# Performance work log

Hardware: AMD Instinct MI355X
Metric: run time of the kernel (lower is better)

## Reference

```python
import jax, jax.numpy as jnp
import numpy as np

N_NODES = 100000
N_EDGES = 400000
IN_DIM = 771
HID = 256
N_GRAPHS = 64
EPS = 1e-5


def setup_inputs() -> dict:
    key = jax.random.key(0)
    ks = jax.random.split(key, 24)
    x = jax.random.normal(ks[0], (N_NODES, IN_DIM), dtype=jnp.float32)
    edge_index = jax.random.randint(ks[1], (2, N_EDGES), 0, N_NODES, dtype=jnp.int64)
    batch = jnp.sort(jax.random.randint(ks[2], (N_NODES,), 0, N_GRAPHS, dtype=jnp.int64))
    inp = {"x": x, "edge_index": edge_index, "batch": batch}
    dims = [IN_DIM, HID, HID]
    ki = 3
    for i, din in enumerate(dims):
        s = 1.0 / np.sqrt(din)
        inp[f"Wl{i}"] = jax.random.normal(ks[ki], (din, HID), dtype=jnp.float32) * s; ki += 1
        inp[f"bl{i}"] = jnp.zeros((HID,), dtype=jnp.float32)
        inp[f"Wr{i}"] = jax.random.normal(ks[ki], (din, HID), dtype=jnp.float32) * s; ki += 1
        inp[f"g{i}"] = jnp.ones((HID,), dtype=jnp.float32)
        inp[f"b{i}"] = jnp.zeros((HID,), dtype=jnp.float32)
    # attention pooling: Linear(HID, HID//2) -> Tanh -> Linear(HID//2, 1)
    inp["Wa1"] = jax.random.normal(ks[ki], (HID, HID // 2), dtype=jnp.float32) * (1.0 / np.sqrt(HID)); ki += 1
    inp["ba1"] = jnp.zeros((HID // 2,), dtype=jnp.float32)
    inp["Wa2"] = jax.random.normal(ks[ki], (HID // 2, 1), dtype=jnp.float32) * (1.0 / np.sqrt(HID // 2)); ki += 1
    inp["ba2"] = jnp.zeros((1,), dtype=jnp.float32)
    # classifier: Linear(HID, HID//2) -> ReLU -> Linear(HID//2, 1)
    inp["Wc1"] = jax.random.normal(ks[ki], (HID, HID // 2), dtype=jnp.float32) * (1.0 / np.sqrt(HID)); ki += 1
    inp["bc1"] = jnp.zeros((HID // 2,), dtype=jnp.float32)
    inp["Wc2"] = jax.random.normal(ks[ki], (HID // 2, 1), dtype=jnp.float32) * (1.0 / np.sqrt(HID // 2)); ki += 1
    inp["bc2"] = jnp.zeros((1,), dtype=jnp.float32)
    return inp


def _sage_layer(h, src, dst, Wl, bl, Wr, g, b):
    # SAGEConv(aggr='mean'): out = lin_l(mean_{j->i} x_j) + lin_r(x_i)
    msum = jax.ops.segment_sum(h[src], dst, num_segments=N_NODES)  # [N, d]
    deg = jax.ops.segment_sum(jnp.ones((src.shape[0],), h.dtype), dst, num_segments=N_NODES)
    agg = msum / jnp.maximum(deg, 1.0)[:, None]
    out = agg @ Wl + bl + h @ Wr
    # BatchNorm1d (training-mode batch stats), eval dropout (identity)
    mean = out.mean(axis=0)
    var = out.var(axis=0)
    out = (out - mean) * jax.lax.rsqrt(var + EPS) * g + b
    return jax.nn.relu(out)


def reference(x, edge_index, batch,
              Wl0, bl0, Wr0, g0, b0,
              Wl1, bl1, Wr1, g1, b1,
              Wl2, bl2, Wr2, g2, b2,
              Wa1, ba1, Wa2, ba2,
              Wc1, bc1, Wc2, bc2):
    src, dst = edge_index[0], edge_index[1]
    h = _sage_layer(x, src, dst, Wl0, bl0, Wr0, g0, b0)
    h = _sage_layer(h, src, dst, Wl1, bl1, Wr1, g1, b1)
    h = _sage_layer(h, src, dst, Wl2, bl2, Wr2, g2, b2)
    # attention pooling: per-graph softmax over node scores, weighted sum
    s = (jnp.tanh(h @ Wa1 + ba1) @ Wa2 + ba2)[:, 0]  # [N]
    smax = jax.ops.segment_max(s, batch, num_segments=N_GRAPHS)
    e = jnp.exp(s - smax[batch])
    denom = jax.ops.segment_sum(e, batch, num_segments=N_GRAPHS)
    w = e / denom[batch]
    pooled = jax.ops.segment_sum(h * w[:, None], batch, num_segments=N_GRAPHS)  # [G, HID]
    out = jax.nn.relu(pooled @ Wc1 + bc1) @ Wc2 + bc2  # [G, 1]
    return out[:, 0]
```

## Files before the change

### kernel.cpp

```cpp
#include <hip/hip_runtime.h>
#include <math.h>
#include <stdint.h>

#define HID 256
#define NGRAPH 64
typedef unsigned short ushort_t;

typedef __attribute__((ext_vector_type(8))) short short8;
typedef __attribute__((ext_vector_type(4))) float f32x4;

__device__ __forceinline__ void split2(float v, ushort_t& h, ushort_t& l) {
  unsigned u = __float_as_uint(v);
  unsigned hr = u + 0x7FFFu + ((u >> 16) & 1u);
  h = (ushort_t)(hr >> 16);
  float hf = __uint_as_float(((unsigned)h) << 16);
  float r = v - hf;
  unsigned u2 = __float_as_uint(r);
  unsigned lr = u2 + 0x7FFFu + ((u2 >> 16) & 1u);
  l = (ushort_t)(lr >> 16);
}

#define GLDS(g, l) \
  __builtin_amdgcn_global_load_lds((const __attribute__((address_space(1))) void*)(g), \
                                   (__attribute__((address_space(3))) void*)(l), 16, 0, 0)

__global__ __launch_bounds__(256) void mfma_gemm512_kernel(
    const ushort_t* __restrict__ Ah, const ushort_t* __restrict__ Al,
    const ushort_t* __restrict__ Bh, const ushort_t* __restrict__ Bl,
    float* __restrict__ C, int Mrows, int Kpad) {
  __shared__ ushort_t lAh[128 * 32];
  __shared__ ushort_t lAl[128 * 32];
  __shared__ ushort_t lBh[128 * 32];
  __shared__ ushort_t lBl[128 * 32];
  const int tid = threadIdx.x;
  const int m0 = blockIdx.y * 128;
  const int n0 = blockIdx.x * 128;
  const int w = tid >> 6, lane = tid & 63;
  const int wm = (w >> 1) * 64, wn = (w & 1) * 64;
  const int col = lane & 15, quad = lane >> 4;

  f32x4 acc[4][4];
#pragma unroll
  for (int i = 0; i < 4; ++i)
#pragma unroll
    for (int j = 0; j < 4; ++j) acc[i][j] = (f32x4)(0.f);

  for (int kt = 0; kt < Kpad; kt += 32) {
#pragma unroll
    for (int j = 0; j < 2; ++j) {
      const int ch = tid + j * 256;
      const int r = ch >> 2, c = ch & 3;
      const size_t goA = (size_t)(m0 + r) * Kpad + kt + c * 8;
      const size_t goB = (size_t)(n0 + r) * Kpad + kt + c * 8;
      GLDS(Ah + goA, &lAh[ch * 8]);
      GLDS(Al + goA, &lAl[ch * 8]);
      GLDS(Bh + goB, &lBh[ch * 8]);
      GLDS(Bl + goB, &lBl[ch * 8]);
    }
    __syncthreads();
    short8 ah[4], al[4], bh[4], bl[4];
#pragma unroll
    for (int i = 0; i < 4; ++i) {
      const int ar = wm + i * 16 + col;
      ah[i] = *(const short8*)&lAh[ar * 32 + quad * 8];
      al[i] = *(const short8*)&lAl[ar * 32 + quad * 8];
      const int br = wn + i * 16 + col;
      bh[i] = *(const short8*)&lBh[br * 32 + quad * 8];
      bl[i] = *(const short8*)&lBl[br * 32 + quad * 8];
    }
    __syncthreads();
#pragma unroll
    for (int i = 0; i < 4; ++i)
#pragma unroll
      for (int j = 0; j < 4; ++j) {
        acc[i][j] = __builtin_amdgcn_mfma_f32_16x16x32_bf16(ah[i], bh[j], acc[i][j], 0, 0, 0);
        acc[i][j] = __builtin_amdgcn_mfma_f32_16x16x32_bf16(ah[i], bl[j], acc[i][j], 0, 0, 0);
        acc[i][j] = __builtin_amdgcn_mfma_f32_16x16x32_bf16(al[i], bh[j], acc[i][j], 0, 0, 0);
      }
  }
#pragma unroll
  for (int i = 0; i < 4; ++i) {
    const int r0 = m0 + wm + i * 16 + quad * 4;
#pragma unroll
    for (int j = 0; j < 4; ++j) {
      const int cc = n0 + wn + j * 16 + col;
#pragma unroll
      for (int r = 0; r < 4; ++r)
        if (r0 + r < Mrows) C[(size_t)(r0 + r) * 512 + cc] = acc[i][j][r];
    }
  }
}

__global__ __launch_bounds__(256) void mfma_att_kernel(
    const ushort_t* __restrict__ Ah, const ushort_t* __restrict__ Al,
    const ushort_t* __restrict__ Bh, const ushort_t* __restrict__ Bl,
    const float* __restrict__ ba1, const float* __restrict__ Wa2,
    const float* __restrict__ ba2, float* __restrict__ S, int Mrows, int Kpad) {
  __shared__ ushort_t lAh[128 * 32];
  __shared__ ushort_t lAl[128 * 32];
  __shared__ ushort_t lBh[128 * 32];
  __shared__ ushort_t lBl[128 * 32];
  __shared__ float sat[128][2];
  const int tid = threadIdx.x;
  const int m0 = blockIdx.y * 128;
  const int w = tid >> 6, lane = tid & 63;
  const int wm = (w >> 1) * 64, wn = (w & 1) * 64;
  const int col = lane & 15, quad = lane >> 4;

  f32x4 acc[4][4];
#pragma unroll
  for (int i = 0; i < 4; ++i)
#pragma unroll
    for (int j = 0; j < 4; ++j) acc[i][j] = (f32x4)(0.f);

  for (int kt = 0; kt < Kpad; kt += 32) {
#pragma unroll
    for (int j = 0; j < 2; ++j) {
      const int ch = tid + j * 256;
      const int r = ch >> 2, c = ch & 3;
      const size_t goA = (size_t)(m0 + r) * Kpad + kt + c * 8;
      const size_t goB = (size_t)r * Kpad + kt + c * 8;
      GLDS(Ah + goA, &lAh[ch * 8]);
      GLDS(Al + goA, &lAl[ch * 8]);
      GLDS(Bh + goB, &lBh[ch * 8]);
      GLDS(Bl + goB, &lBl[ch * 8]);
    }
    __syncthreads();
    short8 ah[4], al[4], bh[4], bl[4];
#pragma unroll
    for (int i = 0; i < 4; ++i) {
      const int ar = wm + i * 16 + col;
      ah[i] = *(const short8*)&lAh[ar * 32 + quad * 8];
      al[i] = *(const short8*)&lAl[ar * 32 + quad * 8];
      const int br = wn + i * 16 + col;
      bh[i] = *(const short8*)&lBh[br * 32 + quad * 8];
      bl[i] = *(const short8*)&lBl[br * 32 + quad * 8];
    }
    __syncthreads();
#pragma unroll
    for (int i = 0; i < 4; ++i)
#pragma unroll
      for (int j = 0; j < 4; ++j) {
        acc[i][j] = __builtin_amdgcn_mfma_f32_16x16x32_bf16(ah[i], bh[j], acc[i][j], 0, 0, 0);
        acc[i][j] = __builtin_amdgcn_mfma_f32_16x16x32_bf16(ah[i], bl[j], acc[i][j], 0, 0, 0);
        acc[i][j] = __builtin_amdgcn_mfma_f32_16x16x32_bf16(al[i], bh[j], acc[i][j], 0, 0, 0);
      }
  }
  float part[4][4];
#pragma unroll
  for (int i = 0; i < 4; ++i)
#pragma unroll
    for (int r = 0; r < 4; ++r) part[i][r] = 0.f;
#pragma unroll
  for (int j = 0; j < 4; ++j) {
    const int cc = wn + j * 16 + col;
    const float a1 = ba1[cc];
    const float w2 = Wa2[cc];
#pragma unroll
    for (int i = 0; i < 4; ++i)
#pragma unroll
      for (int r = 0; r < 4; ++r)
        part[i][r] += tanhf(acc[i][j][r] + a1) * w2;
  }
#pragma unroll
  for (int mask = 1; mask < 16; mask <<= 1)
#pragma unroll
    for (int i = 0; i < 4; ++i)
#pragma unroll
      for (int r = 0; r < 4; ++r) part[i][r] += __shfl_xor(part[i][r], mask, 64);
  if (col == 0) {
#pragma unroll
    for (int i = 0; i < 4; ++i)
#pragma unroll
      for (int r = 0; r < 4; ++r) sat[wm + i * 16 + quad * 4 + r][wn >> 6] = part[i][r];
  }
  __syncthreads();
  if (tid < 128) {
    const int gm = m0 + tid;
    if (gm < Mrows) S[gm] = sat[tid][0] + sat[tid][1] + ba2[0];
  }
}

__global__ __launch_bounds__(256) void convert_x_kernel(
    const float* __restrict__ x, int nrows,
    ushort_t* __restrict__ xh, ushort_t* __restrict__ xl, int K, int Kpad) {
  const int perRow = Kpad / 4;
  const int t = blockIdx.x * blockDim.x + threadIdx.x;
  if (t >= nrows * perRow) return;
  const int r = t / perRow, k0 = (t % perRow) * 4;
  const float* xr = x + (size_t)r * K;
  ushort_t h[4], l[4];
#pragma unroll
  for (int i = 0; i < 4; ++i) {
    const float v = (k0 + i < K) ? xr[k0 + i] : 0.f;
    split2(v, h[i], l[i]);
  }
  const size_t o = (size_t)r * Kpad + k0;
  *(ushort4*)(xh + o) = make_ushort4(h[0], h[1], h[2], h[3]);
  *(ushort4*)(xl + o) = make_ushort4(l[0], l[1], l[2], l[3]);
}

__global__ void convert_wt_kernel(const float* __restrict__ W1, const float* __restrict__ W2,
                                  ushort_t* __restrict__ wth, ushort_t* __restrict__ wtl,
                                  int K, int Kpad, int ntot, int ld) {
  const int t = blockIdx.x * blockDim.x + threadIdx.x;
  if (t >= ntot * Kpad) return;
  const int n = t / Kpad, k = t % Kpad;
  float v = 0.f;
  if (k < K) v = (n < 256) ? W1[(size_t)k * ld + n] : W2[(size_t)k * ld + (n - 256)];
  ushort_t h, l;
  split2(v, h, l);
  wth[t] = h;
  wtl[t] = l;
}

__global__ void deg_count_kernel(const int* __restrict__ dst, int* __restrict__ degi, int nE) {
  int e = blockIdx.x * blockDim.x + threadIdx.x;
  if (e < nE) atomicAdd(&degi[dst[e]], 1);
}

__global__ __launch_bounds__(1024) void scan_kernel(const int* __restrict__ degi,
                                                    int* __restrict__ rowptr, int M) {
  __shared__ int part[1024];
  const int t = threadIdx.x;
  const int chunk = (M + 1023) / 1024;
  const int b0 = min(t * chunk, M);
  const int b1 = min(b0 + chunk, M);
  int s = 0;
  for (int i = b0; i < b1; ++i) s += degi[i];
  part[t] = s;
  __syncthreads();
  for (int off = 1; off < 1024; off <<= 1) {
    int v = (t >= off) ? part[t - off] : 0;
    __syncthreads();
    part[t] += v;
    __syncthreads();
  }
  int ex = (t == 0) ? 0 : part[t - 1];
  for (int i = b0; i < b1; ++i) {
    rowptr[i] = ex;
    ex += degi[i];
  }
  if (t == 1023) rowptr[M] = part[1023];
}

__global__ void fill_kernel(const int* __restrict__ src, const int* __restrict__ dst,
                            int* __restrict__ fill, const int* __restrict__ rowptr,
                            int* __restrict__ csr_src, int nE) {
  int e = blockIdx.x * blockDim.x + threadIdx.x;
  if (e >= nE) return;
  const int d = dst[e];
  const int pos = rowptr[d] + atomicAdd(&fill[d], 1);
  csr_src[pos] = src[e];
}

#define GNB 64
__global__ __launch_bounds__(256) void gather_combine_kernel(
    const float* __restrict__ gbuf,
    const int* __restrict__ rowptr, const int* __restrict__ csr_src,
    const float* __restrict__ bl, float* preBN,
    float* __restrict__ bsum, float* __restrict__ bsumsq, int M) {
  __shared__ float lsum[4][HID];
  __shared__ float lsq[4][HID];
  const int w = threadIdx.x >> 6;
  const int lane = threadIdx.x & 63;
  const float4 blv = ((const float4*)bl)[lane];
  float4 s = make_float4(0.f, 0.f, 0.f, 0.f);
  float4 q = make_float4(0.f, 0.f, 0.f, 0.f);
  const int base = blockIdx.x * GNB;
  for (int it = 0; it < GNB / 4; ++it) {
    const int n = base + it * 4 + w;
    if (n < M) {
      const int e0 = rowptr[n], e1 = rowptr[n + 1];
      float4 acc = make_float4(0.f, 0.f, 0.f, 0.f);
      for (int e = e0; e < e1; ++e) {
        const int sn = csr_src[e];
        const float4 v = ((const float4*)(gbuf + (size_t)sn * 512))[lane];
        acc.x += v.x; acc.y += v.y; acc.z += v.z; acc.w += v.w;
      }
      const float rd = 1.0f / fmaxf((float)(e1 - e0), 1.0f);
      const float4 hv = ((const float4*)(gbuf + (size_t)n * 512 + 256))[lane];
      float4 o;
      o.x = fmaf(acc.x, rd, blv.x + hv.x);
      o.y = fmaf(acc.y, rd, blv.y + hv.y);
      o.z = fmaf(acc.z, rd, blv.z + hv.z);
      o.w = fmaf(acc.w, rd, blv.w + hv.w);
      ((float4*)(preBN + (size_t)n * HID))[lane] = o;
      s.x += o.x; s.y += o.y; s.z += o.z; s.w += o.w;
      q.x = fmaf(o.x, o.x, q.x); q.y = fmaf(o.y, o.y, q.y);
      q.z = fmaf(o.z, o.z, q.z); q.w = fmaf(o.w, o.w, q.w);
    }
  }
  *(float4*)&lsum[w][lane * 4] = s;
  *(float4*)&lsq[w][lane * 4] = q;
  __syncthreads();
  const int c = threadIdx.x;
  const float ts = lsum[0][c] + lsum[1][c] + lsum[2][c] + lsum[3][c];
  const float tq = lsq[0][c] + lsq[1][c] + lsq[2][c] + lsq[3][c];
  atomicAdd(&bsum[c], ts);
  atomicAdd(&bsumsq[c], tq);
}

__global__ __launch_bounds__(256) void bn_apply_relu_convert_kernel(
    const float* __restrict__ preBN, const float* __restrict__ bsum,
    const float* __restrict__ bsumsq, const float* __restrict__ g, const float* __restrict__ b,
    ushort_t* __restrict__ hh, ushort_t* __restrict__ hl, float* __restrict__ hout,
    int M, int n4) {
  __shared__ float s_sc[HID], s_sh[HID];
  {
    const int c = threadIdx.x;
    const float inv = 1.0f / (float)M;
    const float mean = bsum[c] * inv;
    const float var = bsumsq[c] * inv - mean * mean;
    const float sc = g[c] * rsqrtf(var + 1e-5f);
    s_sc[c] = sc;
    s_sh[c] = b[c] - mean * sc;
  }
  __syncthreads();
  const int i = blockIdx.x * blockDim.x + threadIdx.x;
  if (i >= n4) return;
  const int c0 = (i & (HID / 4 - 1)) * 4;
  const float4 v = ((const float4*)preBN)[i];
  float o[4];
  o[0] = fmaxf(fmaf(v.x, s_sc[c0 + 0], s_sh[c0 + 0]), 0.f);
  o[1] = fmaxf(fmaf(v.y, s_sc[c0 + 1], s_sh[c0 + 1]), 0.f);
  o[2] = fmaxf(fmaf(v.z, s_sc[c0 + 2], s_sh[c0 + 2]), 0.f);
  o[3] = fmaxf(fmaf(v.w, s_sc[c0 + 3], s_sh[c0 + 3]), 0.f);
  ushort_t h[4], l[4];
#pragma unroll
  for (int k = 0; k < 4; ++k) split2(o[k], h[k], l[k]);
  ((ushort4*)hh)[i] = make_ushort4(h[0], h[1], h[2], h[3]);
  ((ushort4*)hl)[i] = make_ushort4(l[0], l[1], l[2], l[3]);
  if (hout) ((float4*)hout)[i] = make_float4(o[0], o[1], o[2], o[3]);
}

__device__ __forceinline__ unsigned fflip(float f) {
  unsigned u = __float_as_uint(f);
  return (u & 0x80000000u) ? ~u : (u | 0x80000000u);
}
__device__ __forceinline__ float funflip(unsigned u) {
  return __uint_as_float((u & 0x80000000u) ? (u ^ 0x80000000u) : ~u);
}

__global__ void seg_max_kernel(const float* __restrict__ s, const int* __restrict__ batch,
                               unsigned* __restrict__ gmax, int M) {
  __shared__ unsigned lmax[NGRAPH];
  if (threadIdx.x < NGRAPH) lmax[threadIdx.x] = 0u;
  __syncthreads();
  for (int i = blockIdx.x * blockDim.x + threadIdx.x; i < M; i += gridDim.x * blockDim.x)
    atomicMax(&lmax[batch[i]], fflip(s[i]));
  __syncthreads();
  if (threadIdx.x < NGRAPH && lmax[threadIdx.x] != 0u) atomicMax(&gmax[threadIdx.x], lmax[threadIdx.x]);
}

__global__ void seg_expsum_kernel(const float* __restrict__ s, const int* __restrict__ batch,
                                  const unsigned* __restrict__ gmax, float* __restrict__ e,
                                  float* __restrict__ denom, int M) {
  __shared__ float ld[NGRAPH];
  if (threadIdx.x < NGRAPH) ld[threadIdx.x] = 0.f;
  __syncthreads();
  for (int i = blockIdx.x * blockDim.x + threadIdx.x; i < M; i += gridDim.x * blockDim.x) {
    const int b = batch[i];
    const float v = expf(s[i] - funflip(gmax[b]));
    e[i] = v;
    atomicAdd(&ld[b], v);
  }
  __syncthreads();
  if (threadIdx.x < NGRAPH && ld[threadIdx.x] != 0.f) atomicAdd(&denom[threadIdx.x], ld[threadIdx.x]);
}

#define PNB 16
__global__ __launch_bounds__(256) void pool_kernel(
    const float* __restrict__ h, const float* __restrict__ e, const float* __restrict__ denom,
    const int* __restrict__ batch, float* __restrict__ pooled, int M) {
  const int wid = (blockIdx.x * blockDim.x + threadIdx.x) >> 6;
  const int lane = threadIdx.x & 63;
  const int n0 = wid * PNB;
  if (n0 >= M) return;
  const int n1 = min(n0 + PNB, M);
  float4 acc = make_float4(0.f, 0.f, 0.f, 0.f);
  int cur = batch[n0];
  for (int n = n0; n < n1; ++n) {
    const int b = batch[n];
    if (b != cur) {
      float* o = pooled + (size_t)cur * HID + lane * 4;
      atomicAdd(o + 0, acc.x); atomicAdd(o + 1, acc.y);
      atomicAdd(o + 2, acc.z); atomicAdd(o + 3, acc.w);
      acc = make_float4(0.f, 0.f, 0.f, 0.f);
      cur = b;
    }
    const float w = e[n] / denom[b];
    const float4 v = ((const float4*)(h + (size_t)n * HID))[lane];
    acc.x = fmaf(v.x, w, acc.x); acc.y = fmaf(v.y, w, acc.y);
    acc.z = fmaf(v.z, w, acc.z); acc.w = fmaf(v.w, w, acc.w);
  }
  float* o = pooled + (size_t)cur * HID + lane * 4;
  atomicAdd(o + 0, acc.x); atomicAdd(o + 1, acc.y);
  atomicAdd(o + 2, acc.z); atomicAdd(o + 3, acc.w);
}

__global__ __launch_bounds__(128) void classifier_kernel(
    const float* __restrict__ pooled, const float* __restrict__ Wc1, const float* __restrict__ bc1,
    const float* __restrict__ Wc2, const float* __restrict__ bc2, float* __restrict__ out) {
  __shared__ float red[128];
  const int g = blockIdx.x;
  const int j = threadIdx.x;
  float acc = bc1[j];
  const float* p = pooled + (size_t)g * HID;
  for (int c = 0; c < HID; ++c) acc = fmaf(p[c], Wc1[c * 128 + j], acc);
  red[j] = fmaxf(acc, 0.f) * Wc2[j];
  __syncthreads();
  for (int off = 64; off > 0; off >>= 1) {
    if (j < off) red[j] += red[j + off];
    __syncthreads();
  }
  if (j == 0) out[g] = red[0] + bc2[0];
}

extern "C" void kernel_launch(void* const* d_in, const int* in_sizes, int n_in,
                              void* d_out, int out_size, void* d_ws, size_t ws_size,
                              hipStream_t stream) {
  const float* x = (const float*)d_in[0];
  const int* edge = (const int*)d_in[1];
  const int* batch = (const int*)d_in[2];
  const int M = in_sizes[2];
  const int nE = in_sizes[1] / 2;
  const int IN_DIM = in_sizes[0] / M;
  const int* src = edge;
  const int* dst = edge + nE;

  const int Mpad = ((M + 127) / 128) * 128;
  const int KP0 = ((IN_DIM + 31) / 32) * 32;
  const int mblocks = (M + 127) / 128;

  float* ws = (float*)d_ws;
  float* gbuf = ws;
  float* pbuf = gbuf + (size_t)M * 512;
  float* h32 = pbuf + (size_t)M * HID;
  float* ssc = h32 + (size_t)M * HID;
  float* ew = ssc + M;
  float* bsumA = ew + M;
  unsigned* gmax = (unsigned*)(bsumA + 6 * HID);
  float* denom = (float*)(gmax + NGRAPH);
  float* pooled = denom + NGRAPH;
  int* degi = (int*)(pooled + (size_t)NGRAPH * HID);
  int* filla = degi + M;
  int* rowptr = filla + M;
  int* csr_src = rowptr + M + 1;

  ushort_t* wp = (ushort_t*)(((uintptr_t)(csr_src + nE) + 15) & ~(uintptr_t)15);
  ushort_t* w0h = wp;                 ushort_t* w0l = w0h + (size_t)512 * KP0;
  ushort_t* w1h = w0l + (size_t)512 * KP0;  ushort_t* w1l = w1h + (size_t)512 * HID;
  ushort_t* w2h = w1l + (size_t)512 * HID;  ushort_t* w2l = w2h + (size_t)512 * HID;
  ushort_t* wah = w2l + (size_t)512 * HID;  ushort_t* wal = wah + (size_t)128 * HID;
  ushort_t* cvh = (ushort_t*)(((uintptr_t)(wal + (size_t)128 * HID) + 15) & ~(uintptr_t)15);
  ushort_t* cvl = cvh + (size_t)Mpad * KP0;

  hipMemsetAsync(degi, 0, (size_t)(2 * M) * sizeof(int), stream);
  deg_count_kernel<<<(nE + 255) / 256, 256, 0, stream>>>(dst, degi, nE);
  scan_kernel<<<1, 1024, 0, stream>>>(degi, rowptr, M);
  fill_kernel<<<(nE + 255) / 256, 256, 0, stream>>>(src, dst, filla, rowptr, csr_src, nE);
  hipMemsetAsync(bsumA, 0, (size_t)(6 * HID + 2 * NGRAPH + NGRAPH * HID) * 4, stream);

  {
    const int nt0 = 512 * KP0;
    convert_wt_kernel<<<(nt0 + 255) / 256, 256, 0, stream>>>(
        (const float*)d_in[3], (const float*)d_in[5], w0h, w0l, IN_DIM, KP0, 512, HID);
    const int nt1 = 512 * HID;
    convert_wt_kernel<<<(nt1 + 255) / 256, 256, 0, stream>>>(
        (const float*)d_in[8], (const float*)d_in[10], w1h, w1l, HID, HID, 512, HID);
    convert_wt_kernel<<<(nt1 + 255) / 256, 256, 0, stream>>>(
        (const float*)d_in[13], (const float*)d_in[15], w2h, w2l, HID, HID, 512, HID);
    convert_wt_kernel<<<(128 * HID + 255) / 256, 256, 0, stream>>>(
        (const float*)d_in[18], nullptr, wah, wal, HID, HID, 128, 128);
  }

  {
    const int nt = M * (KP0 / 4);
    convert_x_kernel<<<(nt + 255) / 256, 256, 0, stream>>>(x, M, cvh, cvl, IN_DIM, KP0);
  }

  const int n4 = (int)((size_t)M * HID / 4);
  const ushort_t* WH[3] = {w0h, w1h, w2h};
  const ushort_t* WL[3] = {w0l, w1l, w2l};
  for (int l = 0; l < 3; ++l) {
    const int KP = (l == 0) ? KP0 : HID;
    const float* bl = (const float*)d_in[3 + l * 5 + 1];
    const float* gg = (const float*)d_in[3 + l * 5 + 3];
    const float* bb = (const float*)d_in[3 + l * 5 + 4];
    float* bsum = bsumA + l * 512;
    float* bsumsq = bsum + HID;

    dim3 g(4, mblocks);
    mfma_gemm512_kernel<<<g, 256, 0, stream>>>(cvh, cvl, WH[l], WL[l], gbuf, M, KP);
    gather_combine_kernel<<<(M + GNB - 1) / GNB, 256, 0, stream>>>(
        gbuf, rowptr, csr_src, bl, pbuf, bsum, bsumsq, M);
    bn_apply_relu_convert_kernel<<<(n4 + 255) / 256, 256, 0, stream>>>(
        pbuf, bsum, bsumsq, gg, bb, cvh, cvl, (l == 2) ? h32 : nullptr, M, n4);
  }

  {
    dim3 g(1, mblocks);
    mfma_att_kernel<<<g, 256, 0, stream>>>(
        cvh, cvl, wah, wal, (const float*)d_in[19], (const float*)d_in[20],
        (const float*)d_in[21], ssc, M, HID);
  }
  seg_max_kernel<<<512, 256, 0, stream>>>(ssc, batch, gmax, M);
  seg_expsum_kernel<<<512, 256, 0, stream>>>(ssc, batch, gmax, ew, denom, M);
  {
    const int nwaves = (M + PNB - 1) / PNB;
    pool_kernel<<<(nwaves * 64 + 255) / 256, 256, 0, stream>>>(h32, ew, denom, batch, pooled, M);
  }
  classifier_kernel<<<NGRAPH, 128, 0, stream>>>(
      pooled, (const float*)d_in[22], (const float*)d_in[23],
      (const float*)d_in[24], (const float*)d_in[25], (float*)d_out);
}
```

Before: 2.100 ms.

## Widen GEMM tile to 128x256 with 512 threads and XOR-swizzle LDS layout

The split-bf16 MFMA GEMM now uses 512-thread blocks covering 128x256 output tiles. Each A tile is loaded once per two column halves instead of four, which cuts global traffic for the A operand. LDS chunk indices are XOR-swizzled by row to reduce bank conflicts on the short8 fragment reads. The cost is more LDS per block and fewer blocks in the grid, which may lower occupancy.

```diff
diff --git a/kernel.cpp b/kernel.cpp
--- a/kernel.cpp
+++ b/kernel.cpp
@@ -24,21 +24,25 @@
   __builtin_amdgcn_global_load_lds((const __attribute__((address_space(1))) void*)(g), \
                                    (__attribute__((address_space(3))) void*)(l), 16, 0, 0)
 
-__global__ __launch_bounds__(256) void mfma_gemm512_kernel(
+__global__ __launch_bounds__(512) void mfma_gemm512_kernel(
     const ushort_t* __restrict__ Ah, const ushort_t* __restrict__ Al,
     const ushort_t* __restrict__ Bh, const ushort_t* __restrict__ Bl,
     float* __restrict__ C, int Mrows, int Kpad) {
   __shared__ ushort_t lAh[128 * 32];
   __shared__ ushort_t lAl[128 * 32];
-  __shared__ ushort_t lBh[128 * 32];
-  __shared__ ushort_t lBl[128 * 32];
+  __shared__ ushort_t lBh[256 * 32];
+  __shared__ ushort_t lBl[256 * 32];
   const int tid = threadIdx.x;
   const int m0 = blockIdx.y * 128;
-  const int n0 = blockIdx.x * 128;
+  const int n0 = blockIdx.x * 256;
   const int w = tid >> 6, lane = tid & 63;
-  const int wm = (w >> 1) * 64, wn = (w & 1) * 64;
+  const int wm = (w >> 2) * 64, wn = (w & 3) * 64;
   const int col = lane & 15, quad = lane >> 4;
 
+  const int rA = tid >> 2;
+  const int cA = (tid & 3) ^ ((rA >> 1) & 3);
+  const int rB1 = rA + 128;
+
   f32x4 acc[4][4];
 #pragma unroll
   for (int i = 0; i < 4; ++i)
@@ -46,27 +50,29 @@
     for (int j = 0; j < 4; ++j) acc[i][j] = (f32x4)(0.f);
 
   for (int kt = 0; kt < Kpad; kt += 32) {
-#pragma unroll
-    for (int j = 0; j < 2; ++j) {
-      const int ch = tid + j * 256;
-      const int r = ch >> 2, c = ch & 3;
-      const size_t goA = (size_t)(m0 + r) * Kpad + kt + c * 8;
-      const size_t goB = (size_t)(n0 + r) * Kpad + kt + c * 8;
-      GLDS(Ah + goA, &lAh[ch * 8]);
-      GLDS(Al + goA, &lAl[ch * 8]);
-      GLDS(Bh + goB, &lBh[ch * 8]);
-      GLDS(Bl + goB, &lBl[ch * 8]);
+    {
+      const size_t goA = (size_t)(m0 + rA) * Kpad + kt + cA * 8;
+      GLDS(Ah + goA, &lAh[tid * 8]);
+      GLDS(Al + goA, &lAl[tid * 8]);
+      const size_t goB0 = (size_t)(n0 + rA) * Kpad + kt + cA * 8;
+      GLDS(Bh + goB0, &lBh[tid * 8]);
+      GLDS(Bl + goB0, &lBl[tid * 8]);
+      const size_t goB1 = (size_t)(n0 + rB1) * Kpad + kt + cA * 8;
+      GLDS(Bh + goB1, &lBh[(tid + 512) * 8]);
+      GLDS(Bl + goB1, &lBl[(tid + 512) * 8]);
     }
     __syncthreads();
     short8 ah[4], al[4], bh[4], bl[4];
 #pragma unroll
     for (int i = 0; i < 4; ++i) {
       const int ar = wm + i * 16 + col;
-      ah[i] = *(const short8*)&lAh[ar * 32 + quad * 8];
-      al[i] = *(const short8*)&lAl[ar * 32 + quad * 8];
+      const int sA = ar * 4 + (quad ^ ((ar >> 1) & 3));
+      ah[i] = *(const short8*)&lAh[sA * 8];
+      al[i] = *(const short8*)&lAl[sA * 8];
       const int br = wn + i * 16 + col;
-      bh[i] = *(const short8*)&lBh[br * 32 + quad * 8];
-      bl[i] = *(const short8*)&lBl[br * 32 + quad * 8];
+      const int sB = br * 4 + (quad ^ ((br >> 1) & 3));
+      bh[i] = *(const short8*)&lBh[sB * 8];
+      bl[i] = *(const short8*)&lBl[sB * 8];
     }
     __syncthreads();
 #pragma unroll
@@ -491,8 +497,8 @@
     float* bsum = bsumA + l * 512;
     float* bsumsq = bsum + HID;
 
-    dim3 g(4, mblocks);
-    mfma_gemm512_kernel<<<g, 256, 0, stream>>>(cvh, cvl, WH[l], WL[l], gbuf, M, KP);
+    dim3 g(2, mblocks);
+    mfma_gemm512_kernel<<<g, 512, 0, stream>>>(cvh, cvl, WH[l], WL[l], gbuf, M, KP);
     gather_combine_kernel<<<(M + GNB - 1) / GNB, 256, 0, stream>>>(
         gbuf, rowptr, csr_src, bl, pbuf, bsum, bsumsq, M);
     bn_apply_relu_convert_kernel<<<(n4 + 255) / 256, 256, 0, stream>>>(
```

Result: slower. 2.201 ms (+4.8%).
